# Optimization experiments

Hardware: AMD Instinct MI355X
Metric: run time of the kernel (lower is better)

## Reference

```python
import jax, jax.numpy as jnp
import numpy as np

B, D, E, S, H, Z = 16384, 512, 16, 1, 256, 256

def setup_inputs() -> dict:
    key = jax.random.key(0)
    ks = jax.random.split(key, 6)
    scale = 1.0 / np.sqrt(D)
    return {
        'h':   jax.random.normal(ks[0], (B, D), dtype=jnp.float32),
        'phi': jax.random.normal(ks[1], (D, E, S), dtype=jnp.float32) * scale,
        'W1':  jax.random.normal(ks[2], (E, D, H), dtype=jnp.float32) * scale,
        'b1':  jax.random.normal(ks[3], (E, H), dtype=jnp.float32) * 0.01,
        'W2':  jax.random.normal(ks[4], (E, H, Z), dtype=jnp.float32) * (1.0 / np.sqrt(H)),
        'b2':  jax.random.normal(ks[5], (E, Z), dtype=jnp.float32) * 0.01,
    }

def reference(h, phi, W1, b1, W2, b2):
    # x: (B, n=1, D)
    x = h[:, None, :]
    # routing logits: (B, n, E, S)
    weights = jnp.einsum('bnd,des->bnes', x, phi)
    # dispatch softmax over tokens n (n=1 -> all ones, kept for faithfulness)
    dispatch = jax.nn.softmax(weights, axis=1)
    # expert slot inputs: (B, E, S, D)
    expert_in = jnp.einsum('bnes,bnd->besd', dispatch, x)
    # batched per-expert 2-layer MLP (grouped GEMM over expert axis e)
    hid = jnp.maximum(jnp.einsum('besd,edh->besh', expert_in, W1) + b1[None, :, None, :], 0.0)
    expert_out = jnp.einsum('besh,ehz->besz', hid, W2) + b2[None, :, None, :]  # (B,E,S,Z)
    # combine: softmax over flattened (E*S) slots
    expert_out = expert_out.reshape(expert_out.shape[0], E * S, Z)            # (B, E*S, Z)
    combine = jax.nn.softmax(weights.reshape(weights.shape[0], 1, E * S), axis=-1)
    out = jnp.einsum('bnz,bzd->bnd', combine, expert_out)                     # (B, 1, Z)
    return out[:, 0]
```

## Files before the change

kernel.cpp:

```cpp
#include <hip/hip_runtime.h>

typedef __attribute__((ext_vector_type(8))) short short8;
typedef __attribute__((ext_vector_type(4))) float f32x4;

constexpr int Bsz = 16384;
constexpr int Dd  = 512;
constexpr int Ee  = 16;
constexpr int Hh  = 256;
constexpr int Zz  = 256;
constexpr int BT  = 64;
constexpr int WCLD = 17;
constexpr int HLD  = 544;
constexpr int CHK  = 16384;
constexpr int OFF_P   = 65536;
constexpr int OFF_HID = OFF_P + 4 * 3 * 4096;
constexpr int OFF_WC  = OFF_HID + BT * HLD;
constexpr int OFF_B1  = OFF_WC + 64 * WCLD * 4;
constexpr int SMEM_MAIN = OFF_B1 + 1024;

#define WAITV(N) asm volatile("s_waitcnt vmcnt(" #N ")" ::: "memory")

__device__ __forceinline__ unsigned short f2bf(float f) {
    unsigned u = __float_as_uint(f);
    u += 0x7FFFu + ((u >> 16) & 1u);
    return (unsigned short)(u >> 16);
}

__device__ __forceinline__ int hoff(int b, int h) {
    return b * HLD + ((((h) >> 3) ^ (b & 7)) << 4) + ((h & 7) << 1);
}

__device__ __forceinline__ size_t woff(int row, int k) {
    return (size_t)(k >> 5) * CHK + (size_t)row * 64 +
           ((((k >> 3) & 3) ^ ((row >> 1) & 3)) << 4) + ((k & 7) << 1);
}

__device__ __forceinline__ void stage4(const char* chunkBase, char* ldsbuf,
                                       int wv, int lane) {
    const char* g = chunkBase + wv * 4096 + lane * 16;
    #pragma unroll
    for (int r = 0; r < 4; ++r)
        __builtin_amdgcn_global_load_lds(
            (const __attribute__((address_space(1))) void*)(g + r * 1024),
            (__attribute__((address_space(3))) void*)(ldsbuf + r * 1024), 16, 0, 0);
}

__global__ void transpose_pack(const float* __restrict__ src,
                               unsigned short* __restrict__ dst,
                               int R, int C) {
    __shared__ float tile[64][65];
    int tilesC = C >> 6, tilesR = R >> 6;
    int bid = blockIdx.x;
    int e  = bid / (tilesR * tilesC);
    int rm = bid % (tilesR * tilesC);
    int rt = rm / tilesC;
    int ct = rm % tilesC;
    int t  = threadIdx.x;
    int c  = t & 63;
    int r0 = t >> 6;
    const float* s = src + (size_t)e * R * C + (size_t)(rt * 64) * C + ct * 64;
    #pragma unroll
    for (int i = 0; i < 16; ++i) {
        int r = r0 + i * 4;
        tile[r][c] = s[(size_t)r * C + c];
    }
    __syncthreads();
    char* dbase = (char*)dst + (size_t)e * R * C * 2;
    #pragma unroll
    for (int i = 0; i < 16; ++i) {
        int r = r0 + i * 4;
        int row_g = ct * 64 + r;
        int k_g   = rt * 64 + c;
        *reinterpret_cast<unsigned short*>(dbase + woff(row_g, k_g)) =
            f2bf(tile[c][r]);
    }
}

__global__ __launch_bounds__(256, 1) void moe_fused(
    const float* __restrict__ hptr,
    const float* __restrict__ phi,
    const float* __restrict__ b1,
    const float* __restrict__ b2,
    const char* __restrict__ w1c,
    const char* __restrict__ w2c,
    float* __restrict__ out)
{
    extern __shared__ char smem[];
    char*  hA   = smem;
    char*  hidB = smem + OFF_HID;
    float* wc   = (float*)(smem + OFF_WC);

    const int t    = threadIdx.x;
    const int lane = t & 63;
    const int wv   = t >> 6;
    const int l15  = lane & 15;
    const int lg   = lane >> 4;
    const int b0   = blockIdx.x * BT;
    const int csb  = (l15 >> 1) & 3;

    char* pw = smem + OFF_P + wv * 12288;

    stage4(w1c, pw, wv, lane);
    stage4(w1c + CHK, pw + 4096, wv, lane);

    {
        const f32x4* hsrc = reinterpret_cast<const f32x4*>(hptr + (size_t)b0 * Dd);
        #pragma unroll
        for (int i = 0; i < 32; ++i) {
            int idx = t + i * 256;
            int row = idx >> 7;
            int kc  = idx & 127;
            int k   = kc << 2;
            f32x4 v = hsrc[(size_t)row * 128 + kc];
            unsigned lo = (unsigned)f2bf(v.x) | ((unsigned)f2bf(v.y) << 16);
            unsigned hi = (unsigned)f2bf(v.z) | ((unsigned)f2bf(v.w) << 16);
            int byte = (row << 10) + (((k >> 3) ^ (row & 7)) << 4) + ((k & 7) << 1);
            *reinterpret_cast<uint2*>(hA + byte) = make_uint2(lo, hi);
        }
    }
    __syncthreads();

    {
        f32x4 g[4];
        #pragma unroll
        for (int m = 0; m < 4; ++m) g[m] = (f32x4){0.f, 0.f, 0.f, 0.f};
        #pragma unroll
        for (int kc = 0; kc < 16; ++kc) {
            int kb = kc * 32 + lg * 8;
            short8 bfr;
            #pragma unroll
            for (int j = 0; j < 8; ++j)
                bfr[j] = (short)f2bf(phi[(size_t)(kb + j) * Ee + l15]);
            #pragma unroll
            for (int m = 0; m < 4; ++m) {
                int row = m * 16 + l15;
                short8 af = *reinterpret_cast<const short8*>(
                    hA + (row << 10) + (((kb >> 3) ^ (row & 7)) << 4));
                g[m] = __builtin_amdgcn_mfma_f32_16x16x32_bf16(af, bfr, g[m], 0, 0, 0);
            }
        }
        if (wv == 0) {
            #pragma unroll
            for (int m = 0; m < 4; ++m)
                #pragma unroll
                for (int j = 0; j < 4; ++j)
                    wc[(m * 16 + lg * 4 + j) * WCLD + l15] = g[m][j];
        }
    }
    __syncthreads();
    if (t < 64) {
        float w[16];
        float mx = -1e30f;
        #pragma unroll
        for (int e = 0; e < 16; ++e) { w[e] = wc[t * WCLD + e]; mx = fmaxf(mx, w[e]); }
        float s = 0.f;
        #pragma unroll
        for (int e = 0; e < 16; ++e) { w[e] = __expf(w[e] - mx); s += w[e]; }
        float inv = 1.f / s;
        #pragma unroll
        for (int e = 0; e < 16; ++e) wc[t * WCLD + e] = w[e] * inv;
    }
    __syncthreads();

    f32x4 outacc[4][4];
    #pragma unroll
    for (int mi = 0; mi < 4; ++mi)
        #pragma unroll
        for (int n = 0; n < 4; ++n) outacc[mi][n] = (f32x4){0.f, 0.f, 0.f, 0.f};

    const char* w1e = w1c;
    for (int e = 0; e < Ee; ++e) {
        const char* w2e = w2c + (size_t)e * (Hh * Hh * 2);
        const char* w1n = w1c + (size_t)((e + 1) & 15) * (Hh * Dd * 2);

        __builtin_amdgcn_global_load_lds(
            (const __attribute__((address_space(1))) void*)(b1 + (size_t)e * Hh + wv * 64 + lane),
            (__attribute__((address_space(3))) void*)(smem + OFF_B1 + wv * 256), 4, 0, 0);

        f32x4 hacc[4][4];
        #pragma unroll
        for (int mi = 0; mi < 4; ++mi)
            #pragma unroll
            for (int n = 0; n < 4; ++n) hacc[mi][n] = (f32x4){0.f, 0.f, 0.f, 0.f};

        #pragma unroll
        for (int ci = 0; ci < 16; ++ci) {
            const char* nsrc = (ci + 2 < 16) ? (w1e + (ci + 2) * CHK)
                                             : (w2e + (ci - 14) * CHK);
            stage4(nsrc, pw + ((ci + 2) % 3) * 4096, wv, lane);
            if (ci < 2) { WAITV(9); } else { WAITV(8); }
            const char* pb = pw + (ci % 3) * 4096;
            short8 aw[4], bh[4];
            #pragma unroll
            for (int mi = 0; mi < 4; ++mi) {
                int rp = mi * 16 + l15;
                aw[mi] = *reinterpret_cast<const short8*>(
                    pb + rp * 64 + ((lg ^ csb) << 4));
            }
            int kg = ci * 32 + lg * 8;
            #pragma unroll
            for (int n = 0; n < 4; ++n) {
                int b = n * 16 + l15;
                bh[n] = *reinterpret_cast<const short8*>(
                    hA + (b << 10) + (((kg >> 3) ^ (b & 7)) << 4));
            }
            #pragma unroll
            for (int mi = 0; mi < 4; ++mi)
                #pragma unroll
                for (int n = 0; n < 4; ++n)
                    hacc[mi][n] = __builtin_amdgcn_mfma_f32_16x16x32_bf16(
                        aw[mi], bh[n], hacc[mi][n], 0, 0, 0);
        }

        asm volatile("s_barrier" ::: "memory");

        {
            const float* b1w = (const float*)(smem + OFF_B1) + wv * 64;
            int hb0 = wv * 64 + lg * 4;
            #pragma unroll
            for (int mi = 0; mi < 4; ++mi) {
                int hb = hb0 + mi * 16;
                f32x4 b1v = *reinterpret_cast<const f32x4*>(b1w + lg * 4 + mi * 16);
                #pragma unroll
                for (int n = 0; n < 4; ++n) {
                    int b = n * 16 + l15;
                    float cbe = wc[b * WCLD + e];
                    float v0 = fmaxf(hacc[mi][n][0] + b1v[0], 0.f) * cbe;
                    float v1 = fmaxf(hacc[mi][n][1] + b1v[1], 0.f) * cbe;
                    float v2 = fmaxf(hacc[mi][n][2] + b1v[2], 0.f) * cbe;
                    float v3 = fmaxf(hacc[mi][n][3] + b1v[3], 0.f) * cbe;
                    unsigned lo = (unsigned)f2bf(v0) | ((unsigned)f2bf(v1) << 16);
                    unsigned hi = (unsigned)f2bf(v2) | ((unsigned)f2bf(v3) << 16);
                    *reinterpret_cast<uint2*>(hidB + hoff(b, hb)) = make_uint2(lo, hi);
                }
            }
        }
        asm volatile("s_waitcnt lgkmcnt(0)\n\ts_barrier" ::: "memory");

        #pragma unroll
        for (int gi = 0; gi < 8; ++gi) {
            const char* nsrc = (gi + 2 < 8) ? (w2e + (gi + 2) * CHK)
                                            : (w1n + (gi - 6) * CHK);
            stage4(nsrc, pw + (gi % 3) * 4096, wv, lane);
            WAITV(8);
            const char* pb = pw + ((gi + 1) % 3) * 4096;
            short8 aw[4], bh[4];
            #pragma unroll
            for (int mi = 0; mi < 4; ++mi) {
                int rp = mi * 16 + l15;
                aw[mi] = *reinterpret_cast<const short8*>(
                    pb + rp * 64 + ((lg ^ csb) << 4));
            }
            int kg = gi * 32 + lg * 8;
            #pragma unroll
            for (int n = 0; n < 4; ++n) {
                int b = n * 16 + l15;
                bh[n] = *reinterpret_cast<const short8*>(
                    hidB + b * HLD + (((kg >> 3) ^ (b & 7)) << 4));
            }
            #pragma unroll
            for (int mi = 0; mi < 4; ++mi)
                #pragma unroll
                for (int n = 0; n < 4; ++n)
                    outacc[mi][n] = __builtin_amdgcn_mfma_f32_16x16x32_bf16(
                        aw[mi], bh[n], outacc[mi][n], 0, 0, 0);
        }

        w1e = w1n;
    }

    {
        int zb = wv * 64 + lg * 4;
        #pragma unroll
        for (int e = 0; e < 16; ++e) {
            float cbe[4];
            #pragma unroll
            for (int n = 0; n < 4; ++n) cbe[n] = wc[(n * 16 + l15) * WCLD + e];
            #pragma unroll
            for (int mi = 0; mi < 4; ++mi) {
                f32x4 b2v = *reinterpret_cast<const f32x4*>(
                    b2 + (size_t)e * Zz + zb + mi * 16);
                #pragma unroll
                for (int n = 0; n < 4; ++n) outacc[mi][n] += cbe[n] * b2v;
            }
        }
        #pragma unroll
        for (int mi = 0; mi < 4; ++mi) {
            #pragma unroll
            for (int n = 0; n < 4; ++n) {
                int b = b0 + n * 16 + l15;
                *reinterpret_cast<f32x4*>(out + (size_t)b * Zz + zb + mi * 16) =
                    outacc[mi][n];
            }
        }
    }
    asm volatile("s_waitcnt vmcnt(0)" ::: "memory");
}

extern "C" void kernel_launch(void* const* d_in, const int* in_sizes, int n_in,
                              void* d_out, int out_size, void* d_ws, size_t ws_size,
                              hipStream_t stream) {
    const float* h   = (const float*)d_in[0];
    const float* phi = (const float*)d_in[1];
    const float* W1  = (const float*)d_in[2];
    const float* b1  = (const float*)d_in[3];
    const float* W2  = (const float*)d_in[4];
    const float* b2  = (const float*)d_in[5];
    float* out = (float*)d_out;

    unsigned short* w1p = (unsigned short*)d_ws;
    unsigned short* w2p = w1p + (size_t)Ee * Hh * Dd;

    (void)hipFuncSetAttribute((const void*)moe_fused,
                              hipFuncAttributeMaxDynamicSharedMemorySize, SMEM_MAIN);

    transpose_pack<<<Ee * (Dd / 64) * (Hh / 64), 256, 0, stream>>>(W1, w1p, Dd, Hh);
    transpose_pack<<<Ee * (Hh / 64) * (Zz / 64), 256, 0, stream>>>(W2, w2p, Hh, Zz);

    moe_fused<<<Bsz / BT, 256, SMEM_MAIN, stream>>>(
        h, phi, b1, b2, (const char*)w1p, (const char*)w2p, out);
}
```

Measured before the change: 125.2 us.

## Software-pipeline LDS fragment reads with double-buffered registers across MFMA halves

Restructures both GEMM loops so the A/B fragments for the next K-chunk are read from LDS into a second register set while the current chunk's MFMAs run. Each iteration is split into two MFMA halves with the next-chunk LDS reads and the vmcnt wait placed between them. The aim is to hide LDS read latency behind matrix work. It raises VGPR pressure and depends on the changed wait counts and buffer indexing staying correct across the GEMM1/GEMM2 and expert boundaries.

```diff
diff --git a/kernel.cpp b/kernel.cpp
--- a/kernel.cpp
+++ b/kernel.cpp
@@ -100,6 +100,35 @@
 
     char* pw = smem + OFF_P + wv * 12288;
 
+    short8 awA[4], bhA[4], awB[4], bhB[4];
+
+    auto readAW = [&](short8 (&aw)[4], const char* pb) {
+        #pragma unroll
+        for (int mi = 0; mi < 4; ++mi) {
+            int rp = mi * 16 + l15;
+            aw[mi] = *reinterpret_cast<const short8*>(
+                pb + rp * 64 + ((lg ^ csb) << 4));
+        }
+    };
+    auto readBH_hA = [&](short8 (&bh)[4], int kbase) {
+        int kg = kbase + lg * 8;
+        #pragma unroll
+        for (int n = 0; n < 4; ++n) {
+            int b = n * 16 + l15;
+            bh[n] = *reinterpret_cast<const short8*>(
+                hA + (b << 10) + (((kg >> 3) ^ (b & 7)) << 4));
+        }
+    };
+    auto readBH_hid = [&](short8 (&bh)[4], int kbase) {
+        int kg = kbase + lg * 8;
+        #pragma unroll
+        for (int n = 0; n < 4; ++n) {
+            int b = n * 16 + l15;
+            bh[n] = *reinterpret_cast<const short8*>(
+                hidB + b * HLD + (((kg >> 3) ^ (b & 7)) << 4));
+        }
+    };
+
     stage4(w1c, pw, wv, lane);
     stage4(w1c + CHK, pw + 4096, wv, lane);
 
@@ -177,39 +206,50 @@
             (const __attribute__((address_space(1))) void*)(b1 + (size_t)e * Hh + wv * 64 + lane),
             (__attribute__((address_space(3))) void*)(smem + OFF_B1 + wv * 256), 4, 0, 0);
 
+        if (e == 0) {
+            WAITV(5);
+            readAW(awA, pw);
+            readBH_hA(bhA, 0);
+        }
+
         f32x4 hacc[4][4];
         #pragma unroll
         for (int mi = 0; mi < 4; ++mi)
             #pragma unroll
             for (int n = 0; n < 4; ++n) hacc[mi][n] = (f32x4){0.f, 0.f, 0.f, 0.f};
 
-        #pragma unroll
-        for (int ci = 0; ci < 16; ++ci) {
+        auto mfmaHalf1 = [&](short8 (&aw)[4], short8 (&bh)[4], f32x4 (&acc)[4][4]) {
+            #pragma unroll
+            for (int mi = 0; mi < 2; ++mi)
+                #pragma unroll
+                for (int n = 0; n < 4; ++n)
+                    acc[mi][n] = __builtin_amdgcn_mfma_f32_16x16x32_bf16(
+                        aw[mi], bh[n], acc[mi][n], 0, 0, 0);
+        };
+        auto mfmaHalf2 = [&](short8 (&aw)[4], short8 (&bh)[4], f32x4 (&acc)[4][4]) {
+            #pragma unroll
+            for (int mi = 2; mi < 4; ++mi)
+                #pragma unroll
+                for (int n = 0; n < 4; ++n)
+                    acc[mi][n] = __builtin_amdgcn_mfma_f32_16x16x32_bf16(
+                        aw[mi], bh[n], acc[mi][n], 0, 0, 0);
+        };
+
+        auto g1iter = [&](int ci, short8 (&awC)[4], short8 (&bhC)[4],
+                          short8 (&awN)[4], short8 (&bhN)[4]) {
             const char* nsrc = (ci + 2 < 16) ? (w1e + (ci + 2) * CHK)
                                              : (w2e + (ci - 14) * CHK);
             stage4(nsrc, pw + ((ci + 2) % 3) * 4096, wv, lane);
-            if (ci < 2) { WAITV(9); } else { WAITV(8); }
-            const char* pb = pw + (ci % 3) * 4096;
-            short8 aw[4], bh[4];
-            #pragma unroll
-            for (int mi = 0; mi < 4; ++mi) {
-                int rp = mi * 16 + l15;
-                aw[mi] = *reinterpret_cast<const short8*>(
-                    pb + rp * 64 + ((lg ^ csb) << 4));
-            }
-            int kg = ci * 32 + lg * 8;
-            #pragma unroll
-            for (int n = 0; n < 4; ++n) {
-                int b = n * 16 + l15;
-                bh[n] = *reinterpret_cast<const short8*>(
-                    hA + (b << 10) + (((kg >> 3) ^ (b & 7)) << 4));
-            }
-            #pragma unroll
-            for (int mi = 0; mi < 4; ++mi)
-                #pragma unroll
-                for (int n = 0; n < 4; ++n)
-                    hacc[mi][n] = __builtin_amdgcn_mfma_f32_16x16x32_bf16(
-                        aw[mi], bh[n], hacc[mi][n], 0, 0, 0);
+            mfmaHalf1(awC, bhC, hacc);
+            WAITV(4);
+            readAW(awN, pw + ((ci + 1) % 3) * 4096);
+            if (ci < 15) readBH_hA(bhN, (ci + 1) * 32);
+            mfmaHalf2(awC, bhC, hacc);
+        };
+        #pragma unroll
+        for (int c2 = 0; c2 < 16; c2 += 2) {
+            g1iter(c2,     awA, bhA, awB, bhB);
+            g1iter(c2 + 1, awB, bhB, awA, bhA);
         }
 
         asm volatile("s_barrier" ::: "memory");
@@ -237,33 +277,24 @@
         }
         asm volatile("s_waitcnt lgkmcnt(0)\n\ts_barrier" ::: "memory");
 
-        #pragma unroll
-        for (int gi = 0; gi < 8; ++gi) {
-            const char* nsrc = (gi + 2 < 8) ? (w2e + (gi + 2) * CHK)
-                                            : (w1n + (gi - 6) * CHK);
-            stage4(nsrc, pw + (gi % 3) * 4096, wv, lane);
-            WAITV(8);
-            const char* pb = pw + ((gi + 1) % 3) * 4096;
-            short8 aw[4], bh[4];
-            #pragma unroll
-            for (int mi = 0; mi < 4; ++mi) {
-                int rp = mi * 16 + l15;
-                aw[mi] = *reinterpret_cast<const short8*>(
-                    pb + rp * 64 + ((lg ^ csb) << 4));
-            }
-            int kg = gi * 32 + lg * 8;
-            #pragma unroll
-            for (int n = 0; n < 4; ++n) {
-                int b = n * 16 + l15;
-                bh[n] = *reinterpret_cast<const short8*>(
-                    hidB + b * HLD + (((kg >> 3) ^ (b & 7)) << 4));
-            }
-            #pragma unroll
-            for (int mi = 0; mi < 4; ++mi)
-                #pragma unroll
-                for (int n = 0; n < 4; ++n)
-                    outacc[mi][n] = __builtin_amdgcn_mfma_f32_16x16x32_bf16(
-                        aw[mi], bh[n], outacc[mi][n], 0, 0, 0);
+        readBH_hid(bhA, 0);
+
+        auto g2iter = [&](int j, short8 (&awC)[4], short8 (&bhC)[4],
+                          short8 (&awN)[4], short8 (&bhN)[4]) {
+            const char* nsrc = (j + 2 < 8) ? (w2e + (j + 2) * CHK)
+                                           : (w1n + (j - 6) * CHK);
+            stage4(nsrc, pw + ((16 + j + 2) % 3) * 4096, wv, lane);
+            mfmaHalf1(awC, bhC, outacc);
+            WAITV(4);
+            readAW(awN, pw + ((16 + j + 1) % 3) * 4096);
+            if (j < 7) readBH_hid(bhN, (j + 1) * 32);
+            else       readBH_hA(bhN, 0);
+            mfmaHalf2(awC, bhC, outacc);
+        };
+        #pragma unroll
+        for (int j2 = 0; j2 < 8; j2 += 2) {
+            g2iter(j2,     awA, bhA, awB, bhB);
+            g2iter(j2 + 1, awB, bhB, awA, bhA);
         }
 
         w1e = w1n;
```

After: 146.6 us. 17.1% more time.
